# Optimization experiments

Hardware: AMD Instinct MI355X
Metric: run time of the kernel (lower is better)

## Reference

```python
import jax, jax.numpy as jnp
import numpy as np

# dims
R, N, E = 3, 20000, 250000      # relations, nodes, edges per relation
H, D, DR = 4, 32, 32            # heads, node hidden, relation hidden
RELIN0 = 64                     # relation input dim (layer 0)
IN = H * D                      # node feature dim after projection (128)
NEG = 0.2                       # leaky_relu negative slope


def setup_inputs() -> dict:
    key = jax.random.key(0)
    ks = iter(jax.random.split(key, 40))
    f = lambda *s: 0.05 * jax.random.normal(next(ks), s, jnp.float32)
    return dict(
        x=jax.random.normal(next(ks), (R, N, IN), jnp.float32),
        src=jax.random.randint(next(ks), (R, E), 0, N, jnp.int32),
        dst=jax.random.randint(next(ks), (R, E), 0, N, jnp.int32),
        proj_W=f(IN, IN), proj_b=f(IN),
        rel_emb0=f(R, RELIN0),
        Wn0=f(IN, H * D), Wr0=f(R, RELIN0, H * 2 * D),
        Wp0=f(R, RELIN0, H * DR), bp0=f(R, H * DR),
        Wres0=f(IN, H * D), bres0=f(H * D), resw0=f(1), Wx0=f(R, H, D),
        Wn1=f(IN, H * D), Wr1=f(R, H * DR, H * 2 * D),
        Wp1=f(R, H * DR, H * DR), bp1=f(R, H * DR),
        Wres1=f(IN, H * D), bres1=f(H * D), resw1=f(1), Wx1=f(R, H, D),
        Wnf=f(R, H, D, D), Wrf=f(R, H, DR, D),
    )


def _segment_softmax(e, seg, n):
    # softmax over incoming edges grouped by destination node
    m = jax.ops.segment_max(e, seg, num_segments=n)
    m = jnp.where(jnp.isfinite(m), m, 0.0)
    p = jnp.exp(e - m[seg])
    s = jax.ops.segment_sum(p, seg, num_segments=n)
    return p / (s[seg] + 1e-16)


def _layer(x, relemb, src, dst, Wn, Wr, Wp, bp, Wres, bres, resw, Wx):
    # x: (R, N, IN) relation-specific target node features (eval mode: dropout=identity)
    def conv(x_r, s, d, Wr_r, re_r):
        h = (x_r @ Wn).reshape(N, H, D)              # (N, H, D)
        ra = (re_r @ Wr_r).reshape(H, 2 * D)          # relation attention vector
        e_dst = (h * ra[:, :D]).sum(-1)               # (N, H)
        e_src = (h * ra[:, D:]).sum(-1)               # (N, H)
        e = jax.nn.leaky_relu(e_src[s] + e_dst[d], NEG)  # (E, H)
        a = _segment_softmax(e, d, N)                 # edge softmax per dst node
        msg = jax.ops.segment_sum(h[s] * a[..., None], d, num_segments=N)  # (N, H, D)
        return jax.nn.relu(msg).reshape(N, H * D)
    out = jax.vmap(conv, in_axes=(0, 0, 0, 0, 0))(x, src, dst, Wr, relemb)  # (R, N, H*D)
    # residual gate
    alpha = jax.nn.sigmoid(resw)
    out = out * alpha + (x @ Wres + bres) * (1.0 - alpha)
    # cross-relation attention (all relations share the single dst ntype)
    feats = out.reshape(R, N, H, D)
    def cross(w):  # w: (H, D) per-etype crossing attention weight
        sc = jax.nn.leaky_relu((feats * w).sum(-1, keepdims=True), NEG)  # (R, N, H, 1)
        a = jax.nn.softmax(sc, axis=0)
        return (feats * a).sum(0)                    # (N, H, D)
    out = jax.vmap(cross)(Wx).reshape(R, N, H * D)
    # relation embedding propagation
    relemb = jnp.einsum('ri,rio->ro', relemb, Wp) + bp
    return out, relemb


def reference(x, src, dst, proj_W, proj_b, rel_emb0,
              Wn0, Wr0, Wp0, bp0, Wres0, bres0, resw0, Wx0,
              Wn1, Wr1, Wp1, bp1, Wres1, bres1, resw1, Wx1,
              Wnf, Wrf):
    x = x @ proj_W + proj_b                            # per-ntype projection
    x, re_ = _layer(x, rel_emb0, src, dst, Wn0, Wr0, Wp0, bp0, Wres0, bres0, resw0, Wx0)
    x, re_ = _layer(x, re_, src, dst, Wn1, Wr1, Wp1, bp1, Wres1, bres1, resw1, Wx1)
    # RelationFusing across relation-specific representations
    feats = x.reshape(R, N, H, D)
    rel = re_.reshape(R, H, DR)
    hf = jnp.einsum('rnhd,rhde->rnhe', feats, Wnf)     # per-relation per-head transform
    rp = jnp.einsum('rhc,rhcd->rhd', rel, Wrf)
    sc = jax.nn.softmax(jax.nn.leaky_relu((hf * rp[:, None]).sum(-1, keepdims=True), NEG), axis=0)
    return (hf * sc).sum(0).reshape(N, H * D)          # fused node embeddings
```

## Files before the change

### kernel.cpp

```cpp
#include <hip/hip_runtime.h>
#include <hip/hip_bf16.h>

#define R_ 3
#define N_ 20000
#define NP_ 20096
#define E_ 250000
#define H_ 4
#define D_ 32
#define IN_ 128
#define NEG_ 0.2f

static __device__ __forceinline__ float leaky(float v) { return v >= 0.f ? v : NEG_ * v; }

static __device__ __forceinline__ float red32(float v) {
    #pragma unroll
    for (int m = 16; m > 0; m >>= 1) v += __shfl_xor(v, m, 64);
    return v;
}

__global__ void count_kernel(const int* __restrict__ dst, int* __restrict__ cnt) {
    int i = blockIdx.x * blockDim.x + threadIdx.x;
    if (i < R_ * E_) {
        int r = i / E_;
        atomicAdd(&cnt[r * N_ + dst[i]], 1);
    }
}

__global__ __launch_bounds__(1024)
void scan_kernel(const int* __restrict__ cnt, int* __restrict__ rowptr, int* __restrict__ cursor) {
    const int r = blockIdx.x;
    const int t = threadIdx.x;
    const int CH = 20;
    int local[CH];
    int s = 0;
    int b0 = t * CH;
    #pragma unroll
    for (int i = 0; i < CH; i++) {
        int idx = b0 + i;
        int v = (idx < N_) ? cnt[r * N_ + idx] : 0;
        local[i] = s;
        s += v;
    }
    __shared__ int ts[1024];
    ts[t] = s;
    __syncthreads();
    for (int off = 1; off < 1024; off <<= 1) {
        int v = (t >= off) ? ts[t - off] : 0;
        __syncthreads();
        ts[t] += v;
        __syncthreads();
    }
    int texcl = ts[t] - s;
    #pragma unroll
    for (int i = 0; i < CH; i++) {
        int idx = b0 + i;
        if (idx < N_) {
            int p = texcl + local[i];
            rowptr[r * (N_ + 1) + idx] = p;
            cursor[r * N_ + idx] = p;
        }
    }
    if (t == 1023) rowptr[r * (N_ + 1) + N_] = ts[1023];
}

__global__ void fill_kernel(const int* __restrict__ src, const int* __restrict__ dst,
                            int* __restrict__ cursor, int* __restrict__ csr,
                            int* __restrict__ posmap) {
    int i = blockIdx.x * blockDim.x + threadIdx.x;
    if (i < R_ * E_) {
        int r = i / E_;
        int d = dst[i];
        int pos = atomicAdd(&cursor[r * N_ + d], 1);
        csr[r * E_ + pos] = src[i];
        posmap[i] = pos;
    }
}

__global__ void ra_kernel(const float* __restrict__ re, const float* __restrict__ Wr,
                          float* __restrict__ ra, int relin) {
    int r = blockIdx.x, c = threadIdx.x;
    float a = 0.f;
    for (int i = 0; i < relin; i++) a += re[r * relin + i] * Wr[(r * relin + i) * 256 + c];
    ra[r * 256 + c] = a;
}

__global__ void prop_kernel(const float* __restrict__ re, const float* __restrict__ Wp,
                            const float* __restrict__ bp, float* __restrict__ out, int relin) {
    int r = blockIdx.x, o = threadIdx.x;
    float a = bp[r * 128 + o];
    for (int i = 0; i < relin; i++) a += re[r * relin + i] * Wp[(r * relin + i) * 128 + o];
    out[r * 128 + o] = a;
}

__global__ void rp_kernel(const float* __restrict__ re2, const float* __restrict__ Wrf,
                          float* __restrict__ rp) {
    int r = blockIdx.x, t = threadIdx.x, h = t >> 5, d = t & 31;
    float a = 0.f;
    #pragma unroll
    for (int c = 0; c < 32; c++)
        a += re2[r * 128 + h * 32 + c] * Wrf[(((r * H_ + h) * D_) + c) * D_ + d];
    rp[r * 128 + t] = a;
}

__global__ void combine_W(const float* __restrict__ P, const float* __restrict__ W,
                          float* __restrict__ Wc) {
    const int i = blockIdx.x, j = threadIdx.x;
    float a = 0.f;
    #pragma unroll 8
    for (int k = 0; k < 128; k++) a += P[i * 128 + k] * W[k * 128 + j];
    Wc[i * 128 + j] = a;
}

__global__ void combine_b(const float* __restrict__ pb, const float* __restrict__ W,
                          const float* __restrict__ bin, float* __restrict__ bc) {
    const int j = threadIdx.x;
    float a = bin ? bin[j] : 0.f;
    #pragma unroll 8
    for (int k = 0; k < 128; k++) a += pb[k] * W[k * 128 + j];
    bc[j] = a;
}

__global__ __launch_bounds__(512)
void gemm_dual(const float* __restrict__ X, int ldrows, int nrows,
               const float* __restrict__ Wa, const float* __restrict__ ba,
               float* __restrict__ Ya,
               const float* __restrict__ Wb, const float* __restrict__ bb,
               float* __restrict__ Yb,
               const float* __restrict__ ra, float* __restrict__ esrc,
               float* __restrict__ edst) {
    const int t  = threadIdx.x;
    const int tx = t & 31;
    const int ty = t >> 5;
    const int r  = blockIdx.y;
    const int row0 = blockIdx.x * 128;

    const float* Xrel = X + (size_t)r * ldrows * 128;

    __shared__ float As[32][132];
    __shared__ float Bs[32][256];

    float acc[8][8];
    #pragma unroll
    for (int i = 0; i < 8; i++)
        #pragma unroll
        for (int j = 0; j < 8; j++) acc[i][j] = 0.f;

    const int kq = t & 7;
    for (int kb = 0; kb < 128; kb += 32) {
        __syncthreads();
        #pragma unroll
        for (int j = 0; j < 2; j++) {
            int rowl = (t >> 3) + 64 * j;
            int rowg = row0 + rowl;
            int rowc = rowg < nrows ? rowg : nrows - 1;
            float4 v = *(const float4*)&Xrel[(size_t)rowc * 128 + kb + kq * 4];
            As[kq * 4 + 0][rowl] = v.x;
            As[kq * 4 + 1][rowl] = v.y;
            As[kq * 4 + 2][rowl] = v.z;
            As[kq * 4 + 3][rowl] = v.w;
        }
        #pragma unroll
        for (int j = 0; j < 4; j++) {
            int fi = t + 512 * j;
            int kk = fi >> 6;
            int colq = fi & 63;
            float4 v = (colq < 32)
                ? *(const float4*)&Wa[(size_t)(kb + kk) * 128 + colq * 4]
                : *(const float4*)&Wb[(size_t)(kb + kk) * 128 + (colq - 32) * 4];
            *(float4*)&Bs[kk][colq * 4] = v;
        }
        __syncthreads();
        #pragma unroll 8
        for (int k = 0; k < 32; k++) {
            float a[8], b[8];
            *(float4*)&a[0] = *(const float4*)&As[k][ty * 8];
            *(float4*)&a[4] = *(const float4*)&As[k][ty * 8 + 4];
            *(float4*)&b[0] = *(const float4*)&Bs[k][tx * 4];
            *(float4*)&b[4] = *(const float4*)&Bs[k][tx * 4 + 128];
            #pragma unroll
            for (int i = 0; i < 8; i++)
                #pragma unroll
                for (int j = 0; j < 8; j++) acc[i][j] += a[i] * b[j];
        }
    }

    const int col0 = tx * 4;
    float baq[4], bbq[4];
    #pragma unroll
    for (int j = 0; j < 4; j++) {
        baq[j] = ba[col0 + j];
        bbq[j] = bb ? bb[col0 + j] : 0.f;
    }
    #pragma unroll
    for (int i = 0; i < 8; i++)
        #pragma unroll
        for (int j = 0; j < 4; j++) {
            acc[i][j]     += baq[j];
            acc[i][4 + j] += bbq[j];
        }

    float* Yar = Ya + (size_t)r * NP_ * 128;
    float* Ybr = Yb + (size_t)r * NP_ * 128;
    const int hh = tx >> 3;
    float rad[4], ras[4];
    #pragma unroll
    for (int j = 0; j < 4; j++) {
        int c = (tx & 7) * 4 + j;
        rad[j] = ra[(r * H_ + hh) * 64 + c];
        ras[j] = ra[(r * H_ + hh) * 64 + 32 + c];
    }
    #pragma unroll
    for (int i = 0; i < 8; i++) {
        int row = row0 + ty * 8 + i;
        float4 oa = {acc[i][0], acc[i][1], acc[i][2], acc[i][3]};
        float4 ob = {acc[i][4], acc[i][5], acc[i][6], acc[i][7]};
        *(float4*)&Yar[(size_t)row * 128 + col0] = oa;
        *(float4*)&Ybr[(size_t)row * 128 + col0] = ob;
        float vd = 0.f, vs = 0.f;
        #pragma unroll
        for (int j = 0; j < 4; j++) { vd += acc[i][4 + j] * rad[j]; vs += acc[i][4 + j] * ras[j]; }
        vd += __shfl_xor(vd, 1); vd += __shfl_xor(vd, 2); vd += __shfl_xor(vd, 4);
        vs += __shfl_xor(vs, 1); vs += __shfl_xor(vs, 2); vs += __shfl_xor(vs, 4);
        if ((tx & 7) == 0) {
            edst[((size_t)r * NP_ + row) * 4 + hh] = vd;
            esrc[((size_t)r * NP_ + row) * 4 + hh] = vs;
        }
    }
}

__global__ void edgep_kernel(const int* __restrict__ src, const int* __restrict__ dst,
                             const int* __restrict__ posmap,
                             const float* __restrict__ esrc, const float* __restrict__ edst,
                             float4* __restrict__ pbuf) {
    int i = blockIdx.x * blockDim.x + threadIdx.x;
    if (i >= R_ * E_) return;
    int r = i / E_;
    int s = src[i], d = dst[i];
    const float4 es = *(const float4*)&esrc[((size_t)r * NP_ + s) * 4];
    const float4 ed = *(const float4*)&edst[((size_t)r * NP_ + d) * 4];
    float4 p;
    p.x = __expf(leaky(es.x + ed.x));
    p.y = __expf(leaky(es.y + ed.y));
    p.z = __expf(leaky(es.z + ed.z));
    p.w = __expf(leaky(es.w + ed.w));
    pbuf[(size_t)r * E_ + posmap[i]] = p;
}

__global__ __launch_bounds__(128)
void aggregate(const float* __restrict__ hbuf, const float* __restrict__ pbuf,
               const int* __restrict__ rowptr, const int* __restrict__ csr,
               const float* __restrict__ resw, float* __restrict__ io) {
    const int n = blockIdx.x, r = blockIdx.y;
    const int t = threadIdx.x;
    const int lane32 = t & 31;
    const int slot = t >> 5;
    const int h = lane32 >> 3;
    const int beg = rowptr[r * (N_ + 1) + n];
    const int end = rowptr[r * (N_ + 1) + n + 1];

    float4 acc = {0.f, 0.f, 0.f, 0.f};
    float psum = 0.f;
    for (int j0 = beg; j0 < end; j0 += 4) {
        int j = j0 + slot;
        bool valid = j < end;
        int jc = valid ? j : beg;
        int s = csr[r * E_ + jc];
        float p = valid ? pbuf[((size_t)r * E_ + j) * 4 + h] : 0.f;
        const float4 hv = *(const float4*)&hbuf[((size_t)r * NP_ + s) * 128 + lane32 * 4];
        acc.x += p * hv.x; acc.y += p * hv.y; acc.z += p * hv.z; acc.w += p * hv.w;
        psum += p;
    }

    __shared__ float4 sacc[4][32];
    __shared__ float spsum[4][32];
    sacc[slot][lane32] = acc;
    spsum[slot][lane32] = psum;
    __syncthreads();
    if (t < 32) {
        float4 a0 = sacc[0][t], a1 = sacc[1][t], a2 = sacc[2][t], a3 = sacc[3][t];
        float ps = spsum[0][t] + spsum[1][t] + spsum[2][t] + spsum[3][t];
        float inv = 1.f / (ps + 1e-16f);
        float alpha = 1.f / (1.f + __expf(-resw[0]));
        float4* iop = (float4*)&io[((size_t)r * NP_ + n) * 128 + t * 4];
        float4 res = *iop;
        float4 o;
        o.x = fmaxf((a0.x + a1.x + a2.x + a3.x) * inv, 0.f) * alpha + res.x * (1.f - alpha);
        o.y = fmaxf((a0.y + a1.y + a2.y + a3.y) * inv, 0.f) * alpha + res.y * (1.f - alpha);
        o.z = fmaxf((a0.z + a1.z + a2.z + a3.z) * inv, 0.f) * alpha + res.z * (1.f - alpha);
        o.w = fmaxf((a0.w + a1.w + a2.w + a3.w) * inv, 0.f) * alpha + res.w * (1.f - alpha);
        *iop = o;
    }
}

__global__ __launch_bounds__(128)
void cross_kernel(const float* __restrict__ fin, const float* __restrict__ Wx,
                  float* __restrict__ fout) {
    const int n = blockIdx.x, t = threadIdx.x;
    float f[3];
    #pragma unroll
    for (int r = 0; r < 3; r++) f[r] = fin[((size_t)r * NP_ + n) * 128 + t];
    #pragma unroll
    for (int k = 0; k < 3; k++) {
        float w = Wx[k * 128 + t];
        float s[3];
        #pragma unroll
        for (int r = 0; r < 3; r++) s[r] = leaky(red32(f[r] * w));
        float mx = fmaxf(s[0], fmaxf(s[1], s[2]));
        float a0 = __expf(s[0] - mx), a1 = __expf(s[1] - mx), a2 = __expf(s[2] - mx);
        float den = a0 + a1 + a2;
        fout[((size_t)k * NP_ + n) * 128 + t] = (f[0] * a0 + f[1] * a1 + f[2] * a2) / den;
    }
}

__global__ __launch_bounds__(128)
void fuse_kernel(const float* __restrict__ fin, const float* __restrict__ Wnf,
                 const float* __restrict__ rp, float* __restrict__ out) {
    const int n = blockIdx.x, t = threadIdx.x, h = t >> 5, e = t & 31;
    __shared__ float sf[3][128];
    #pragma unroll
    for (int r = 0; r < 3; r++) sf[r][t] = fin[((size_t)r * NP_ + n) * 128 + t];
    __syncthreads();
    float hf[3];
    #pragma unroll
    for (int r = 0; r < 3; r++) {
        float a = 0.f;
        #pragma unroll
        for (int d = 0; d < 32; d++)
            a += sf[r][h * 32 + d] * Wnf[(((r * H_ + h) * D_) + d) * D_ + e];
        hf[r] = a;
    }
    float s[3];
    #pragma unroll
    for (int r = 0; r < 3; r++) s[r] = leaky(red32(hf[r] * rp[(r * H_ + h) * D_ + e]));
    float mx = fmaxf(s[0], fmaxf(s[1], s[2]));
    float a0 = __expf(s[0] - mx), a1 = __expf(s[1] - mx), a2 = __expf(s[2] - mx);
    float den = a0 + a1 + a2;
    out[(size_t)n * 128 + t] = (hf[0] * a0 + hf[1] * a1 + hf[2] * a2) / den;
}

extern "C" void kernel_launch(void* const* d_in, const int* in_sizes, int n_in,
                              void* d_out, int out_size, void* d_ws, size_t ws_size,
                              hipStream_t stream) {
    const float* x        = (const float*)d_in[0];
    const int*   src      = (const int*)d_in[1];
    const int*   dst      = (const int*)d_in[2];
    const float* proj_W   = (const float*)d_in[3];
    const float* proj_b   = (const float*)d_in[4];
    const float* rel_emb0 = (const float*)d_in[5];
    const float* Wn0      = (const float*)d_in[6];
    const float* Wr0      = (const float*)d_in[7];
    const float* Wp0      = (const float*)d_in[8];
    const float* bp0      = (const float*)d_in[9];
    const float* Wres0    = (const float*)d_in[10];
    const float* bres0    = (const float*)d_in[11];
    const float* resw0    = (const float*)d_in[12];
    const float* Wx0      = (const float*)d_in[13];
    const float* Wn1      = (const float*)d_in[14];
    const float* Wr1      = (const float*)d_in[15];
    const float* Wp1      = (const float*)d_in[16];
    const float* bp1      = (const float*)d_in[17];
    const float* Wres1    = (const float*)d_in[18];
    const float* bres1    = (const float*)d_in[19];
    const float* resw1    = (const float*)d_in[20];
    const float* Wx1      = (const float*)d_in[21];
    const float* Wnf      = (const float*)d_in[22];
    const float* Wrf      = (const float*)d_in[23];

    char* ws = (char*)d_ws;
    size_t off = 0;
    auto alloc = [&](size_t bytes) { char* p = ws + off; off = (off + bytes + 255) & ~(size_t)255; return p; };
    const size_t BIG = (size_t)R_ * NP_ * 128 * sizeof(float);
    float* bufA  = (float*)alloc(BIG);
    float* bufB  = (float*)alloc(BIG);
    float* hbuf  = (float*)alloc(BIG);
    float* pbuf  = (float*)alloc((size_t)R_ * E_ * 4 * sizeof(float));
    int*   posmap= (int*)alloc((size_t)R_ * E_ * sizeof(int));
    float* esrc  = (float*)alloc((size_t)R_ * NP_ * H_ * sizeof(float));
    float* edst  = (float*)alloc((size_t)R_ * NP_ * H_ * sizeof(float));
    int*   cnt   = (int*)alloc((size_t)R_ * N_ * sizeof(int));
    int*   cursor= (int*)alloc((size_t)R_ * N_ * sizeof(int));
    int*   rowptr= (int*)alloc((size_t)R_ * (N_ + 1) * sizeof(int));
    int*   csr   = (int*)alloc((size_t)R_ * E_ * sizeof(int));
    float* remb1 = (float*)alloc((size_t)R_ * 128 * sizeof(float));
    float* remb2 = (float*)alloc((size_t)R_ * 128 * sizeof(float));
    float* ra0   = (float*)alloc((size_t)R_ * 256 * sizeof(float));
    float* ra1   = (float*)alloc((size_t)R_ * 256 * sizeof(float));
    float* rpb   = (float*)alloc((size_t)R_ * 128 * sizeof(float));
    float* Wres0c= (float*)alloc(128 * 128 * sizeof(float));
    float* Wn0c  = (float*)alloc(128 * 128 * sizeof(float));
    float* bres0c= (float*)alloc(128 * sizeof(float));
    float* bn0c  = (float*)alloc(128 * sizeof(float));

    hipMemsetAsync(cnt, 0, (size_t)R_ * N_ * sizeof(int), stream);
    const int EB = (R_ * E_ + 255) / 256;
    count_kernel<<<EB, 256, 0, stream>>>(dst, cnt);
    scan_kernel<<<R_, 1024, 0, stream>>>(cnt, rowptr, cursor);
    fill_kernel<<<EB, 256, 0, stream>>>(src, dst, cursor, csr, posmap);

    ra_kernel<<<R_, 256, 0, stream>>>(rel_emb0, Wr0, ra0, 64);
    prop_kernel<<<R_, 128, 0, stream>>>(rel_emb0, Wp0, bp0, remb1, 64);
    ra_kernel<<<R_, 256, 0, stream>>>(remb1, Wr1, ra1, 128);
    prop_kernel<<<R_, 128, 0, stream>>>(remb1, Wp1, bp1, remb2, 128);
    rp_kernel<<<R_, 128, 0, stream>>>(remb2, Wrf, rpb);

    combine_W<<<128, 128, 0, stream>>>(proj_W, Wres0, Wres0c);
    combine_b<<<1, 128, 0, stream>>>(proj_b, Wres0, bres0, bres0c);
    combine_W<<<128, 128, 0, stream>>>(proj_W, Wn0, Wn0c);
    combine_b<<<1, 128, 0, stream>>>(proj_b, Wn0, nullptr, bn0c);

    const dim3 GT(NP_ / 128, R_);
    gemm_dual<<<GT, 512, 0, stream>>>(x, N_, N_, Wres0c, bres0c, bufA,
                                      Wn0c, bn0c, hbuf, ra0, esrc, edst);
    edgep_kernel<<<EB, 256, 0, stream>>>(src, dst, posmap, esrc, edst, (float4*)pbuf);
    aggregate<<<dim3(N_, R_), 128, 0, stream>>>(hbuf, pbuf, rowptr, csr, resw0, bufA);
    cross_kernel<<<N_, 128, 0, stream>>>(bufA, Wx0, bufB);
    gemm_dual<<<GT, 512, 0, stream>>>(bufB, NP_, NP_, Wres1, bres1, bufA,
                                      Wn1, nullptr, hbuf, ra1, esrc, edst);
    edgep_kernel<<<EB, 256, 0, stream>>>(src, dst, posmap, esrc, edst, (float4*)pbuf);
    aggregate<<<dim3(N_, R_), 128, 0, stream>>>(hbuf, pbuf, rowptr, csr, resw1, bufA);
    cross_kernel<<<N_, 128, 0, stream>>>(bufA, Wx1, bufB);
    fuse_kernel<<<N_, 128, 0, stream>>>(bufB, Wnf, rpb, (float*)d_out);
}
```

Before: 659.4 us.

## Fuse edge softmax numerator into aggregation and merge small prep kernels

Drops the separate edge-probability kernel and its pbuf/posmap buffers. The aggregation kernel now computes exp(leaky(esrc[s]+edst[n])) inline from the per-node attention scalars. This removes a pass over all edges, a scattered write and the posmap store in fill_kernel, at the cost of an extra gathered read of esrc per edge in aggregation. It also merges the ra/prop and combine_W/combine_b launches into fewer kernels to cut launch overhead.

After: 563.2 us. 14.6% less time.

```diff
diff --git a/kernel.cpp b/kernel.cpp
--- a/kernel.cpp
+++ b/kernel.cpp
@@ -64,32 +64,34 @@
 }
 
 __global__ void fill_kernel(const int* __restrict__ src, const int* __restrict__ dst,
-                            int* __restrict__ cursor, int* __restrict__ csr,
-                            int* __restrict__ posmap) {
+                            int* __restrict__ cursor, int* __restrict__ csr) {
     int i = blockIdx.x * blockDim.x + threadIdx.x;
     if (i < R_ * E_) {
         int r = i / E_;
         int d = dst[i];
         int pos = atomicAdd(&cursor[r * N_ + d], 1);
         csr[r * E_ + pos] = src[i];
-        posmap[i] = pos;
-    }
-}
-
-__global__ void ra_kernel(const float* __restrict__ re, const float* __restrict__ Wr,
-                          float* __restrict__ ra, int relin) {
-    int r = blockIdx.x, c = threadIdx.x;
-    float a = 0.f;
-    for (int i = 0; i < relin; i++) a += re[r * relin + i] * Wr[(r * relin + i) * 256 + c];
-    ra[r * 256 + c] = a;
-}
-
-__global__ void prop_kernel(const float* __restrict__ re, const float* __restrict__ Wp,
-                            const float* __restrict__ bp, float* __restrict__ out, int relin) {
-    int r = blockIdx.x, o = threadIdx.x;
-    float a = bp[r * 128 + o];
-    for (int i = 0; i < relin; i++) a += re[r * relin + i] * Wp[(r * relin + i) * 128 + o];
-    out[r * 128 + o] = a;
+    }
+}
+
+__global__ void relprep_kernel(const float* __restrict__ re, const float* __restrict__ Wr,
+                               float* __restrict__ ra, const float* __restrict__ Wp,
+                               const float* __restrict__ bp, float* __restrict__ remb,
+                               int relin) {
+    const int r = blockIdx.x;
+    if (blockIdx.y == 0) {
+        const int c = threadIdx.x;
+        float a = 0.f;
+        #pragma unroll 8
+        for (int i = 0; i < relin; i++) a += re[r * relin + i] * Wr[(r * relin + i) * 256 + c];
+        ra[r * 256 + c] = a;
+    } else if (threadIdx.x < 128) {
+        const int o = threadIdx.x;
+        float a = bp[r * 128 + o];
+        #pragma unroll 8
+        for (int i = 0; i < relin; i++) a += re[r * relin + i] * Wp[(r * relin + i) * 128 + o];
+        remb[r * 128 + o] = a;
+    }
 }
 
 __global__ void rp_kernel(const float* __restrict__ re2, const float* __restrict__ Wrf,
@@ -102,22 +104,25 @@
     rp[r * 128 + t] = a;
 }
 
-__global__ void combine_W(const float* __restrict__ P, const float* __restrict__ W,
-                          float* __restrict__ Wc) {
-    const int i = blockIdx.x, j = threadIdx.x;
-    float a = 0.f;
-    #pragma unroll 8
-    for (int k = 0; k < 128; k++) a += P[i * 128 + k] * W[k * 128 + j];
-    Wc[i * 128 + j] = a;
-}
-
-__global__ void combine_b(const float* __restrict__ pb, const float* __restrict__ W,
-                          const float* __restrict__ bin, float* __restrict__ bc) {
+__global__ void combine_kernel(const float* __restrict__ P, const float* __restrict__ pb,
+                               const float* __restrict__ W0, const float* __restrict__ b0,
+                               const float* __restrict__ W1,
+                               float* __restrict__ Wc0, float* __restrict__ bc0,
+                               float* __restrict__ Wc1, float* __restrict__ bc1) {
+    const float* W = blockIdx.y ? W1 : W0;
     const int j = threadIdx.x;
-    float a = bin ? bin[j] : 0.f;
-    #pragma unroll 8
-    for (int k = 0; k < 128; k++) a += pb[k] * W[k * 128 + j];
-    bc[j] = a;
+    if (blockIdx.x < 128) {
+        const int i = blockIdx.x;
+        float a = 0.f;
+        #pragma unroll 8
+        for (int k = 0; k < 128; k++) a += P[i * 128 + k] * W[k * 128 + j];
+        (blockIdx.y ? Wc1 : Wc0)[i * 128 + j] = a;
+    } else {
+        float a = blockIdx.y ? 0.f : b0[j];
+        #pragma unroll 8
+        for (int k = 0; k < 128; k++) a += pb[k] * W[k * 128 + j];
+        (blockIdx.y ? bc1 : bc0)[j] = a;
+    }
 }
 
 __global__ __launch_bounds__(512)
@@ -228,28 +233,11 @@
     }
 }
 
-__global__ void edgep_kernel(const int* __restrict__ src, const int* __restrict__ dst,
-                             const int* __restrict__ posmap,
-                             const float* __restrict__ esrc, const float* __restrict__ edst,
-                             float4* __restrict__ pbuf) {
-    int i = blockIdx.x * blockDim.x + threadIdx.x;
-    if (i >= R_ * E_) return;
-    int r = i / E_;
-    int s = src[i], d = dst[i];
-    const float4 es = *(const float4*)&esrc[((size_t)r * NP_ + s) * 4];
-    const float4 ed = *(const float4*)&edst[((size_t)r * NP_ + d) * 4];
-    float4 p;
-    p.x = __expf(leaky(es.x + ed.x));
-    p.y = __expf(leaky(es.y + ed.y));
-    p.z = __expf(leaky(es.z + ed.z));
-    p.w = __expf(leaky(es.w + ed.w));
-    pbuf[(size_t)r * E_ + posmap[i]] = p;
-}
-
 __global__ __launch_bounds__(128)
-void aggregate(const float* __restrict__ hbuf, const float* __restrict__ pbuf,
-               const int* __restrict__ rowptr, const int* __restrict__ csr,
-               const float* __restrict__ resw, float* __restrict__ io) {
+void aggregate(const float* __restrict__ hbuf, const float* __restrict__ esrc,
+               const float* __restrict__ edst, const int* __restrict__ rowptr,
+               const int* __restrict__ csr, const float* __restrict__ resw,
+               float* __restrict__ io) {
     const int n = blockIdx.x, r = blockIdx.y;
     const int t = threadIdx.x;
     const int lane32 = t & 31;
@@ -257,6 +245,7 @@
     const int h = lane32 >> 3;
     const int beg = rowptr[r * (N_ + 1) + n];
     const int end = rowptr[r * (N_ + 1) + n + 1];
+    const float ed = edst[((size_t)r * NP_ + n) * 4 + h];
 
     float4 acc = {0.f, 0.f, 0.f, 0.f};
     float psum = 0.f;
@@ -265,7 +254,8 @@
         bool valid = j < end;
         int jc = valid ? j : beg;
         int s = csr[r * E_ + jc];
-        float p = valid ? pbuf[((size_t)r * E_ + j) * 4 + h] : 0.f;
+        float es = esrc[((size_t)r * NP_ + s) * 4 + h];
+        float p = valid ? __expf(leaky(es + ed)) : 0.f;
         const float4 hv = *(const float4*)&hbuf[((size_t)r * NP_ + s) * 128 + lane32 * 4];
         acc.x += p * hv.x; acc.y += p * hv.y; acc.z += p * hv.z; acc.w += p * hv.w;
         psum += p;
@@ -373,8 +363,6 @@
     float* bufA  = (float*)alloc(BIG);
     float* bufB  = (float*)alloc(BIG);
     float* hbuf  = (float*)alloc(BIG);
-    float* pbuf  = (float*)alloc((size_t)R_ * E_ * 4 * sizeof(float));
-    int*   posmap= (int*)alloc((size_t)R_ * E_ * sizeof(int));
     float* esrc  = (float*)alloc((size_t)R_ * NP_ * H_ * sizeof(float));
     float* edst  = (float*)alloc((size_t)R_ * NP_ * H_ * sizeof(float));
     int*   cnt   = (int*)alloc((size_t)R_ * N_ * sizeof(int));
@@ -395,29 +383,23 @@
     const int EB = (R_ * E_ + 255) / 256;
     count_kernel<<<EB, 256, 0, stream>>>(dst, cnt);
     scan_kernel<<<R_, 1024, 0, stream>>>(cnt, rowptr, cursor);
-    fill_kernel<<<EB, 256, 0, stream>>>(src, dst, cursor, csr, posmap);
-
-    ra_kernel<<<R_, 256, 0, stream>>>(rel_emb0, Wr0, ra0, 64);
-    prop_kernel<<<R_, 128, 0, stream>>>(rel_emb0, Wp0, bp0, remb1, 64);
-    ra_kernel<<<R_, 256, 0, stream>>>(remb1, Wr1, ra1, 128);
-    prop_kernel<<<R_, 128, 0, stream>>>(remb1, Wp1, bp1, remb2, 128);
+    fill_kernel<<<EB, 256, 0, stream>>>(src, dst, cursor, csr);
+
+    relprep_kernel<<<dim3(R_, 2), 256, 0, stream>>>(rel_emb0, Wr0, ra0, Wp0, bp0, remb1, 64);
+    relprep_kernel<<<dim3(R_, 2), 256, 0, stream>>>(remb1, Wr1, ra1, Wp1, bp1, remb2, 128);
     rp_kernel<<<R_, 128, 0, stream>>>(remb2, Wrf, rpb);
 
-    combine_W<<<128, 128, 0, stream>>>(proj_W, Wres0, Wres0c);
-    combine_b<<<1, 128, 0, stream>>>(proj_b, Wres0, bres0, bres0c);
-    combine_W<<<128, 128, 0, stream>>>(proj_W, Wn0, Wn0c);
-    combine_b<<<1, 128, 0, stream>>>(proj_b, Wn0, nullptr, bn0c);
+    combine_kernel<<<dim3(129, 2), 128, 0, stream>>>(proj_W, proj_b, Wres0, bres0, Wn0,
+                                                     Wres0c, bres0c, Wn0c, bn0c);
 
     const dim3 GT(NP_ / 128, R_);
     gemm_dual<<<GT, 512, 0, stream>>>(x, N_, N_, Wres0c, bres0c, bufA,
                                       Wn0c, bn0c, hbuf, ra0, esrc, edst);
-    edgep_kernel<<<EB, 256, 0, stream>>>(src, dst, posmap, esrc, edst, (float4*)pbuf);
-    aggregate<<<dim3(N_, R_), 128, 0, stream>>>(hbuf, pbuf, rowptr, csr, resw0, bufA);
+    aggregate<<<dim3(N_, R_), 128, 0, stream>>>(hbuf, esrc, edst, rowptr, csr, resw0, bufA);
     cross_kernel<<<N_, 128, 0, stream>>>(bufA, Wx0, bufB);
     gemm_dual<<<GT, 512, 0, stream>>>(bufB, NP_, NP_, Wres1, bres1, bufA,
                                       Wn1, nullptr, hbuf, ra1, esrc, edst);
-    edgep_kernel<<<EB, 256, 0, stream>>>(src, dst, posmap, esrc, edst, (float4*)pbuf);
-    aggregate<<<dim3(N_, R_), 128, 0, stream>>>(hbuf, pbuf, rowptr, csr, resw1, bufA);
+    aggregate<<<dim3(N_, R_), 128, 0, stream>>>(hbuf, esrc, edst, rowptr, csr, resw1, bufA);
     cross_kernel<<<N_, 128, 0, stream>>>(bufA, Wx1, bufB);
     fuse_kernel<<<N_, 128, 0, stream>>>(bufB, Wnf, rpb, (float*)d_out);
 }
```
